# Kernel tuning notes

Hardware: AMD Instinct MI355X
Metric: run time of the kernel (lower is better)

The kernel has to match this reference:

```python
import jax, jax.numpy as jnp
import numpy as np
from jax import lax

SEQ, BSZ = 64, 32
NTOK, NINP, NHID, NLAYERS = 50000, 512, 1024, 2
BN_EPS = 1e-5


def setup_inputs() -> dict:
    key = jax.random.key(0)
    ks = jax.random.split(key, 12)
    s = 0.05
    return {
        "input_ids": jax.random.randint(ks[0], (SEQ, BSZ), 0, NTOK),
        "hx": jnp.zeros((NLAYERS, BSZ, NHID), jnp.float32),
        "cx": jnp.zeros((NLAYERS, BSZ, NHID), jnp.float32),
        "emb_w": jax.random.normal(ks[1], (NTOK, NINP), jnp.float32) * 0.01,
        "Wih0": jax.random.normal(ks[2], (4 * NHID, NINP), jnp.float32) * s,
        "Whh0": jax.random.normal(ks[3], (4 * NHID, NHID), jnp.float32) * s,
        "bih0": jnp.zeros((4 * NHID,), jnp.float32),
        "bhh0": jnp.zeros((4 * NHID,), jnp.float32),
        "Wih1": jax.random.normal(ks[4], (4 * NHID, NHID), jnp.float32) * s,
        "Whh1": jax.random.normal(ks[5], (4 * NHID, NHID), jnp.float32) * s,
        "bih1": jnp.zeros((4 * NHID,), jnp.float32),
        "bhh1": jnp.zeros((4 * NHID,), jnp.float32),
        "Wp": jax.random.normal(ks[6], (NINP, NHID), jnp.float32) * s,
        "bp": jnp.zeros((NINP,), jnp.float32),
        "Wd": jax.random.normal(ks[7], (NTOK, NINP), jnp.float32) * 0.01,
        "bd": jnp.zeros((NTOK,), jnp.float32),
    }


def _lstm_cell(x, h, c, Wih, Whh, bih, bhh):
    # torch.nn.LSTMCell math; gates packed as [i, f, g, o]
    gates = x @ Wih.T + bih + h @ Whh.T + bhh  # [B, 4H]
    i, f, g, o = jnp.split(gates, 4, axis=-1)
    i = jax.nn.sigmoid(i)
    f = jax.nn.sigmoid(f)
    g = jnp.tanh(g)
    o = jax.nn.sigmoid(o)
    c2 = f * c + i * g
    h2 = o * jnp.tanh(c2)
    return h2, c2


def reference(input_ids, hx, cx, emb_w, Wih0, Whh0, bih0, bhh0,
              Wih1, Whh1, bih1, bhh1, Wp, bp, Wd, bd):
    # eval mode: drop / internal_drop / rdrop are identity; rmask == 1
    emb = emb_w[input_ids]  # [S, B, ninp]
    layers = ((Wih0, Whh0, bih0, bhh0), (Wih1, Whh1, bih1, bhh1))

    def step(carry, x_t):
        h, c = carry  # each [nlayers, B, H]
        hi = x_t
        hs, cs = [], []
        for j in range(NLAYERS):
            Wih, Whh, bih, bhh = layers[j]
            hj, cj = _lstm_cell(hi, h[j], c[j], Wih, Whh, bih, bhh)
            hs.append(hj)
            cs.append(cj)
            hi = hj
        return (jnp.stack(hs, 0), jnp.stack(cs, 0)), hi

    (hxf, cxf), out = lax.scan(step, (hx, cx), emb)  # out: [S, B, H]
    flat = out.reshape(-1, NHID)  # [S*B, H]
    # predictor: Linear -> BatchNorm1d (eval: running_mean=0, running_var=1,
    # gamma=1, beta=0) -> Tanh
    pre = flat @ Wp.T + bp
    p = jnp.tanh(pre * (1.0 / jnp.sqrt(jnp.float32(1.0 + BN_EPS))))
    decoded = p @ Wd.T + bd  # [S*B, ntoken]
    return decoded.reshape(SEQ, BSZ, NTOK), (hxf, cxf)
```

## Files before the change

kernel.cpp:

```cpp
#include <hip/hip_runtime.h>
#include <hip/hip_bf16.h>

using bf16 = __hip_bfloat16;
typedef __attribute__((ext_vector_type(8))) short short8;
typedef __attribute__((ext_vector_type(4))) float f32x4;

#define MFMA_BF16(A,B,C) __builtin_amdgcn_mfma_f32_16x16x32_bf16((A),(B),(C),0,0,0)

static __device__ __forceinline__ unsigned bf16bits(float f) {
  union { bf16 h; unsigned short u; } cv; cv.h = __float2bfloat16(f); return cv.u;
}

static __device__ __forceinline__ void gload16(const void* g, void* l) {
  __builtin_amdgcn_global_load_lds(
      (const __attribute__((address_space(1))) void*)g,
      (__attribute__((address_space(3))) void*)l, 16, 0, 0);
}

template<int EPI>
__global__ __launch_bounds__(256)
void gemm_bt(const bf16* __restrict__ A, const bf16* __restrict__ B,
             const float* __restrict__ bias1, const float* __restrict__ bias2,
             float* __restrict__ Cf, bf16* __restrict__ Cb,
             int M, int N, int K, int Nreal)
{
  __shared__ __align__(1024) bf16 As[128*32];
  __shared__ __align__(1024) bf16 Bs[128*32];
  const int tid  = threadIdx.x;
  const int wave = tid >> 6, lane = tid & 63;
  const int wr = wave >> 1, wc = wave & 1;
  const int row0 = blockIdx.y * 128;
  const int col0 = blockIdx.x * 128;

  f32x4 acc[4][4];
  #pragma unroll
  for (int m = 0; m < 4; ++m)
    #pragma unroll
    for (int n = 0; n < 4; ++n) { f32x4 z = {0.f,0.f,0.f,0.f}; acc[m][n] = z; }

  const int r_sub = lane >> 2;
  const int kc    = lane & 3;

  for (int k0 = 0; k0 < K; k0 += 32) {
    __syncthreads();
    #pragma unroll
    for (int j = 0; j < 2; ++j) {
      const int rb = wave*32 + j*16;
      gload16(A + (size_t)(row0 + rb + r_sub)*K + k0 + kc*8,
              (void*)((char*)As + (size_t)rb*64));
      gload16(B + (size_t)(col0 + rb + r_sub)*K + k0 + kc*8,
              (void*)((char*)Bs + (size_t)rb*64));
    }
    __syncthreads();

    short8 af[4], bfv[4];
    #pragma unroll
    for (int m = 0; m < 4; ++m)
      af[m] = *(const short8*)(As + (wr*64 + m*16 + (lane&15))*32 + (lane>>4)*8);
    #pragma unroll
    for (int n = 0; n < 4; ++n)
      bfv[n] = *(const short8*)(Bs + (wc*64 + n*16 + (lane&15))*32 + (lane>>4)*8);
    #pragma unroll
    for (int m = 0; m < 4; ++m)
      #pragma unroll
      for (int n = 0; n < 4; ++n)
        acc[m][n] = MFMA_BF16(af[m], bfv[n], acc[m][n]);
  }

  const float BN_SCALE = 0.9999950000374997f;
  #pragma unroll
  for (int m = 0; m < 4; ++m) {
    const int rg0 = row0 + wr*64 + m*16 + ((lane>>4)<<2);
    #pragma unroll
    for (int n = 0; n < 4; ++n) {
      const int cg = col0 + wc*64 + n*16 + (lane&15);
      if (EPI == 2) {
        const int bq = cg >> 4, q = cg & 15;
        const int orig = (q>>2)*1024 + bq*4 + (q&3);
        const float bb = bias1[orig] + bias2[orig];
        #pragma unroll
        for (int j = 0; j < 4; ++j) {
          const int row = rg0 + j;
          Cf[((size_t)bq*64 + (row>>5))*512 + (size_t)(row&31)*16 + q]
              = acc[m][n][j] + bb;
        }
      } else if (cg < Nreal) {
        float bb = 0.f;
        if (bias1) bb += bias1[cg];
        if (bias2) bb += bias2[cg];
        #pragma unroll
        for (int j = 0; j < 4; ++j) {
          float v = acc[m][n][j] + bb;
          v = tanhf(v * BN_SCALE);
          Cb[(size_t)(rg0+j)*Nreal + cg] = __float2bfloat16(v);
        }
      }
    }
  }
}

__global__ __launch_bounds__(512, 2)
void gemm_dec(const bf16* __restrict__ A, const bf16* __restrict__ B,
              const float* __restrict__ bias, float* __restrict__ C,
              int M, int N, int K, int Nreal)
{
  __shared__ __align__(1024) bf16 As[2*256*32];
  __shared__ __align__(1024) bf16 Bs[2*256*32];
  const int tid  = threadIdx.x;
  const int wave = tid >> 6, lane = tid & 63;
  const int wr = wave >> 2, wc = wave & 3;
  const int row0 = blockIdx.y * 256;
  const int col0 = blockIdx.x * 256;

  f32x4 acc[8][4];
  #pragma unroll
  for (int m = 0; m < 8; ++m)
    #pragma unroll
    for (int n = 0; n < 4; ++n) { f32x4 z = {0.f,0.f,0.f,0.f}; acc[m][n] = z; }

  const int r_sub = lane >> 2;
  const int kc    = lane & 3;

  auto STAGE = [&](int sl, int k0) {
    #pragma unroll
    for (int j = 0; j < 2; ++j) {
      const int rb = wave*32 + j*16;
      gload16(A + (size_t)(row0 + rb + r_sub)*K + k0 + kc*8,
              (void*)((char*)As + (size_t)sl*16384 + (size_t)rb*64));
      gload16(B + (size_t)(col0 + rb + r_sub)*K + k0 + kc*8,
              (void*)((char*)Bs + (size_t)sl*16384 + (size_t)rb*64));
    }
  };

  const int NT = K >> 5;
  STAGE(0, 0);
  if (NT > 1) STAGE(1, 32);

  for (int kk = 0; kk < NT; ++kk) {
    const int cur = kk & 1;
    if (kk == NT - 1) asm volatile("s_waitcnt vmcnt(0)" ::: "memory");
    else              asm volatile("s_waitcnt vmcnt(4)" ::: "memory");
    __builtin_amdgcn_sched_barrier(0);
    __builtin_amdgcn_s_barrier();

    const bf16* Ab = As + (size_t)cur*8192;
    const bf16* Bb = Bs + (size_t)cur*8192;
    short8 af[8], bfv[4];
    #pragma unroll
    for (int m = 0; m < 8; ++m)
      af[m] = *(const short8*)(Ab + (wr*128 + m*16 + (lane&15))*32 + (lane>>4)*8);
    #pragma unroll
    for (int n = 0; n < 4; ++n)
      bfv[n] = *(const short8*)(Bb + (wc*64 + n*16 + (lane&15))*32 + (lane>>4)*8);
    #pragma unroll
    for (int m = 0; m < 8; ++m)
      #pragma unroll
      for (int n = 0; n < 4; ++n)
        acc[m][n] = MFMA_BF16(af[m], bfv[n], acc[m][n]);

    asm volatile("s_waitcnt lgkmcnt(0)" ::: "memory");
    __builtin_amdgcn_sched_barrier(0);
    __builtin_amdgcn_s_barrier();
    if (kk + 2 < NT) STAGE(cur, (kk + 2) * 32);
  }

  #pragma unroll
  for (int m = 0; m < 8; ++m) {
    const int rg0 = row0 + wr*128 + m*16 + ((lane>>4)<<2);
    #pragma unroll
    for (int n = 0; n < 4; ++n) {
      const int cg = col0 + wc*64 + n*16 + (lane&15);
      if (cg < Nreal) {
        const float bb = bias[cg];
        #pragma unroll
        for (int j = 0; j < 4; ++j)
          __builtin_nontemporal_store(acc[m][n][j] + bb,
                                      C + (size_t)(rg0+j)*Nreal + cg);
      }
    }
  }
}

__global__ __launch_bounds__(256, 1)
void k_lstm_persist(const bf16* __restrict__ hinit, const float* __restrict__ cx,
                    const bf16* __restrict__ Wpack, const float* __restrict__ g0p,
                    const float* __restrict__ bih1, const float* __restrict__ bhh1,
                    bf16* __restrict__ h0_all, bf16* __restrict__ h1_all,
                    float* __restrict__ tail, unsigned* __restrict__ flags)
{
  const int b    = blockIdx.x;
  const int tid  = threadIdx.x;
  const int wave = tid >> 6, lane = tid & 63;

  __shared__ __align__(1024) bf16 Wlds[96*512];
  __shared__ float P[4][2][32][20];

  const bf16* wbase = Wpack + (size_t)b * 96 * 512;
  #pragma unroll
  for (int it = 0; it < 24; ++it) {
    const int chunk = it*4 + wave;
    gload16(wbase + (size_t)chunk*512 + lane*8,
            (void*)((char*)Wlds + (size_t)chunk*1024));
  }

  const int layer = tid >> 7;
  const int cell  = tid & 127;
  const int r     = cell >> 2;
  const int hc    = cell & 3;
  const int col   = b*4 + hc;
  float creg = cx[(size_t)layer*32768 + (size_t)r*1024 + col];
  float bsum[4];
  #pragma unroll
  for (int g = 0; g < 4; ++g)
    bsum[g] = (layer == 1) ? (bih1[g*1024 + col] + bhh1[g*1024 + col]) : 0.f;

  const int arow = lane & 15;
  const int koff = (lane >> 4) * 8;

  const unsigned* fp0 = flags + (lane*4+0)*32;
  const unsigned* fp1 = flags + (lane*4+1)*32;
  const unsigned* fp2 = flags + (lane*4+2)*32;
  const unsigned* fp3 = flags + (lane*4+3)*32;

  __syncthreads();

  for (int s = 0; s < 65; ++s) {
    const bf16* hA = (s == 0) ? hinit           : h0_all + (size_t)(s-1)*32768;
    const bf16* hB = (s <= 1) ? (hinit + 32768) : h1_all + (size_t)(s-2)*32768;

    short8 a0[8], a1[8], c0[8], c1[8];
    #pragma unroll
    for (int i = 0; i < 8; ++i) {
      const int kb = wave*256 + i*32 + koff;
      a0[i] = *(const short8*)(hA + (size_t)arow*1024      + kb);
      a1[i] = *(const short8*)(hA + (size_t)(arow+16)*1024 + kb);
      c0[i] = *(const short8*)(hB + (size_t)arow*1024      + kb);
      c1[i] = *(const short8*)(hB + (size_t)(arow+16)*1024 + kb);
    }
    float gpre[4] = {0.f, 0.f, 0.f, 0.f};
    if (layer == 0 && s < 64) {
      const float* gr = g0p + ((size_t)(b*64 + s)*32 + r)*16;
      #pragma unroll
      for (int g = 0; g < 4; ++g) gpre[g] = gr[g*4 + hc];
    }

    f32x4 z = {0.f,0.f,0.f,0.f};
    f32x4 acc00 = z, acc01 = z, acc10 = z, acc11 = z;
    #pragma unroll
    for (int i = 0; i < 8; ++i) {
      const int ks = wave*8 + i;
      short8 w0 = *(const short8*)(Wlds + ((size_t)(     ks)*64 + lane)*8);
      short8 w1 = *(const short8*)(Wlds + ((size_t)(32 + ks)*64 + lane)*8);
      short8 w2 = *(const short8*)(Wlds + ((size_t)(64 + ks)*64 + lane)*8);
      acc00 = MFMA_BF16(a0[i], w0, acc00);
      acc01 = MFMA_BF16(a1[i], w0, acc01);
      acc10 = MFMA_BF16(a0[i], w1, acc10);
      acc11 = MFMA_BF16(a1[i], w1, acc11);
      acc10 = MFMA_BF16(c0[i], w2, acc10);
      acc11 = MFMA_BF16(c1[i], w2, acc11);
    }

    #pragma unroll
    for (int j = 0; j < 4; ++j) {
      const int pr = (lane >> 4)*4 + j;
      P[wave][0][pr     ][lane & 15] = acc00[j];
      P[wave][0][pr + 16][lane & 15] = acc01[j];
      P[wave][1][pr     ][lane & 15] = acc10[j];
      P[wave][1][pr + 16][lane & 15] = acc11[j];
    }
    __syncthreads();

    const int t = s - layer;
    if (t >= 0 && t < 64) {
      float v[4];
      #pragma unroll
      for (int g = 0; g < 4; ++g) {
        const int j = g*4 + hc;
        v[g] = P[0][layer][r][j] + P[1][layer][r][j]
             + P[2][layer][r][j] + P[3][layer][r][j] + bsum[g] + gpre[g];
      }
      const float iv = 1.f/(1.f + expf(-v[0]));
      const float fv = 1.f/(1.f + expf(-v[1]));
      const float gv = tanhf(v[2]);
      const float ov = 1.f/(1.f + expf(-v[3]));
      creg = fv*creg + iv*gv;
      const float hn = ov*tanhf(creg);
      unsigned hu  = bf16bits(hn);
      unsigned p01 = hu | ((unsigned)__shfl_xor((int)hu, 1) << 16);
      unsigned p23 = (unsigned)__shfl_xor((int)p01, 2);
      if (hc == 0) {
        bf16* hp = (layer ? h1_all : h0_all) + (size_t)t*32768 + (size_t)r*1024 + b*4;
        unsigned long long v64 = (unsigned long long)p01
                               | ((unsigned long long)p23 << 32);
        __hip_atomic_store((unsigned long long*)hp, v64,
                           __ATOMIC_RELAXED, __HIP_MEMORY_SCOPE_AGENT);
      }
      if (t == 63) {
        tail[(size_t)layer*32768 + (size_t)r*1024 + col]         = hn;
        tail[65536 + (size_t)layer*32768 + (size_t)r*1024 + col] = creg;
      }
    }
    if (s == 64) break;

    __syncthreads();
    if (tid == 0) {
      asm volatile("global_store_dword %0, %1, off sc0 sc1\n\t"
                   "s_waitcnt vmcnt(0)"
                   :: "v"(flags + b*32), "v"((unsigned)(s + 1)) : "memory");
    }
    if (wave == 0) {
      const unsigned su = (unsigned)s;
      for (;;) {
        unsigned v0, v1, v2, v3;
        asm volatile("global_load_dword %0, %1, off sc0 sc1" : "=v"(v0) : "v"(fp0));
        asm volatile("global_load_dword %0, %1, off sc0 sc1" : "=v"(v1) : "v"(fp1));
        asm volatile("global_load_dword %0, %1, off sc0 sc1" : "=v"(v2) : "v"(fp2));
        asm volatile("global_load_dword %0, %1, off sc0 sc1" : "=v"(v3) : "v"(fp3));
        asm volatile("s_waitcnt vmcnt(0)" ::: "memory");
        bool ok = (v0 > su) & (v1 > su) & (v2 > su) & (v3 > su);
        if (__all(ok)) break;
        __builtin_amdgcn_s_sleep(1);
      }
    }
    __syncthreads();
    asm volatile("" ::: "memory");
    __builtin_amdgcn_sched_barrier(0);
  }
}

__global__ __launch_bounds__(256)
void k_pack(const float* __restrict__ Whh0, const float* __restrict__ Wih1,
            const float* __restrict__ Whh1, bf16* __restrict__ Wpack)
{
  const int b = blockIdx.x;
  #pragma unroll 4
  for (int it = 0; it < 24; ++it) {
    const int idx = it*256 + threadIdx.x;
    const int chunkp = idx >> 6;
    const int l = idx & 63;
    const int p = chunkp >> 5, c = chunkp & 31;
    const float* W = (p == 0) ? Whh0 : (p == 1 ? Wih1 : Whh1);
    const int j = l & 15;
    const int row = (j>>2)*1024 + b*4 + (j&3);
    const int k = c*32 + (l>>4)*8;
    const float* src = W + (size_t)row*1024 + k;
    bf16* dst = Wpack + ((size_t)(b*96 + chunkp)*64 + l)*8;
    #pragma unroll
    for (int q = 0; q < 8; ++q) dst[q] = __float2bfloat16(src[q]);
  }
}

__global__ void k_cvt(const float* __restrict__ s, bf16* __restrict__ d, long n) {
  long i = (long)blockIdx.x*blockDim.x + threadIdx.x;
  if (i < n) d[i] = __float2bfloat16(s[i]);
}

__global__ void k_cvt_perm(const float* __restrict__ src, bf16* __restrict__ dst) {
  const int n = blockIdx.x;
  const int orig = ((n>>2)&3)*1024 + (n>>4)*4 + (n&3);
  const float4 v = ((const float4*)(src + (size_t)orig*512))[threadIdx.x];
  bf16* d = dst + (size_t)n*512 + threadIdx.x*4;
  d[0] = __float2bfloat16(v.x); d[1] = __float2bfloat16(v.y);
  d[2] = __float2bfloat16(v.z); d[3] = __float2bfloat16(v.w);
}

__global__ void k_cvt_pad(const float* __restrict__ s, bf16* __restrict__ d,
                          long n, long nrows_real, int rowlen) {
  long i = (long)blockIdx.x*blockDim.x + threadIdx.x;
  if (i < n) {
    long r = i / rowlen;
    d[i] = (r < nrows_real) ? __float2bfloat16(s[i]) : __float2bfloat16(0.f);
  }
}

__global__ void k_init(const float* __restrict__ hx, bf16* __restrict__ hinit,
                       unsigned* __restrict__ flags) {
  int i = blockIdx.x*blockDim.x + threadIdx.x;
  if (i < 8192) flags[i] = 0u;
  if (i < 65536) hinit[i] = __float2bfloat16(hx[i]);
}

__global__ void k_embed(const int* __restrict__ ids, const float* __restrict__ emb_w,
                        bf16* __restrict__ out) {
  const int row = blockIdx.x;
  const int tok = ids[row];
  const float4 v = ((const float4*)(emb_w + (size_t)tok*512))[threadIdx.x];
  bf16* d = out + (size_t)row*512 + threadIdx.x*4;
  d[0] = __float2bfloat16(v.x); d[1] = __float2bfloat16(v.y);
  d[2] = __float2bfloat16(v.z); d[3] = __float2bfloat16(v.w);
}

extern "C" void kernel_launch(void* const* d_in, const int* in_sizes, int n_in,
                              void* d_out, int out_size, void* d_ws, size_t ws_size,
                              hipStream_t stream) {
  const int*   ids  = (const int*)d_in[0];
  const float* hx   = (const float*)d_in[1];
  const float* cx   = (const float*)d_in[2];
  const float* embw = (const float*)d_in[3];
  const float* Wih0 = (const float*)d_in[4];
  const float* Whh0 = (const float*)d_in[5];
  const float* bih0 = (const float*)d_in[6];
  const float* bhh0 = (const float*)d_in[7];
  const float* Wih1 = (const float*)d_in[8];
  const float* Whh1 = (const float*)d_in[9];
  const float* bih1 = (const float*)d_in[10];
  const float* bhh1 = (const float*)d_in[11];
  const float* Wp   = (const float*)d_in[12];
  const float* bp   = (const float*)d_in[13];
  const float* Wd   = (const float*)d_in[14];
  const float* bd   = (const float*)d_in[15];
  float* out = (float*)d_out;

  char* w = (char*)d_ws;
  bf16* Wih0b = (bf16*)w; w += 4096l*512*2;
  bf16* Wpack = (bf16*)w; w += 256l*96*64*8*2;
  bf16* Wpb   = (bf16*)w; w += 512l*1024*2;
  bf16* Wdb   = (bf16*)w; w += 50176l*512*2;
  bf16* embb  = (bf16*)w; w += 2048l*512*2;
  float* g0p  = (float*)w; w += 2048l*4096*4;
  bf16* h0a   = (bf16*)w; w += 2048l*1024*2;
  bf16* h1a   = (bf16*)w; w += 2048l*1024*2;
  bf16* hinit = (bf16*)w; w += 2l*32*1024*2;
  bf16* pb    = (bf16*)w; w += 2048l*512*2;
  unsigned* flags = (unsigned*)w; w += 8192*4;

  k_cvt_perm<<<4096, 128, 0, stream>>>(Wih0, Wih0b);
  k_cvt<<<(512l*1024 + 255)/256, 256, 0, stream>>>(Wp, Wpb, 512l*1024);
  k_cvt_pad<<<(50176l*512 + 255)/256, 256, 0, stream>>>(Wd, Wdb, 50176l*512, 50000, 512);
  k_init<<<256, 256, 0, stream>>>(hx, hinit, flags);
  k_embed<<<2048, 128, 0, stream>>>(ids, embw, embb);
  k_pack<<<256, 256, 0, stream>>>(Whh0, Wih1, Whh1, Wpack);

  gemm_bt<2><<<dim3(32, 16), 256, 0, stream>>>(
      embb, Wih0b, bih0, bhh0, g0p, nullptr, 2048, 4096, 512, 4096);

  float* tail = out + 102400000l;
  k_lstm_persist<<<256, 256, 0, stream>>>(hinit, cx, Wpack, g0p, bih1, bhh1,
                                          h0a, h1a, tail, flags);

  gemm_bt<1><<<dim3(4, 16), 256, 0, stream>>>(
      h1a, Wpb, bp, nullptr, nullptr, pb, 2048, 512, 1024, 512);

  gemm_dec<<<dim3(196, 8), 512, 0, stream>>>(
      pb, Wdb, bd, out, 2048, 50176, 512, 50000);
}
```

Measured before the change: 713.2 us.

## Fold weight conversions into persistent LSTM kernel to overlap with recurrence

Drops the separate k_pack, k_cvt and k_cvt_pad launches. The persistent LSTM kernel now converts its recurrent weights from fp32 straight into LDS, and at each timestep spreads the conversion of the decoder and projection weights to bf16 across all blocks. This is meant to hide the large Wd conversion behind the latency-bound recurrence and remove the Wpack round trip through memory. The cost is extra global traffic and VALU work inside every recurrent step, which could lengthen the critical path between flag syncs.

```diff
diff --git a/kernel.cpp b/kernel.cpp
--- a/kernel.cpp
+++ b/kernel.cpp
@@ -183,8 +183,11 @@
 
 __global__ __launch_bounds__(256, 1)
 void k_lstm_persist(const bf16* __restrict__ hinit, const float* __restrict__ cx,
-                    const bf16* __restrict__ Wpack, const float* __restrict__ g0p,
+                    const float* __restrict__ Whh0, const float* __restrict__ Wih1,
+                    const float* __restrict__ Whh1, const float* __restrict__ g0p,
                     const float* __restrict__ bih1, const float* __restrict__ bhh1,
+                    const float* __restrict__ Wd, const float* __restrict__ Wp,
+                    bf16* __restrict__ Wdb, bf16* __restrict__ Wpb,
                     bf16* __restrict__ h0_all, bf16* __restrict__ h1_all,
                     float* __restrict__ tail, unsigned* __restrict__ flags)
 {
@@ -195,12 +198,25 @@
   __shared__ __align__(1024) bf16 Wlds[96*512];
   __shared__ float P[4][2][32][20];
 
-  const bf16* wbase = Wpack + (size_t)b * 96 * 512;
   #pragma unroll
   for (int it = 0; it < 24; ++it) {
-    const int chunk = it*4 + wave;
-    gload16(wbase + (size_t)chunk*512 + lane*8,
-            (void*)((char*)Wlds + (size_t)chunk*1024));
+    const int idx = it*256 + tid;
+    const int chunkp = idx >> 6;
+    const int l = idx & 63;
+    const int p = chunkp >> 5, c = chunkp & 31;
+    const float* W = (p == 0) ? Whh0 : (p == 1 ? Wih1 : Whh1);
+    const int j = l & 15;
+    const int row = (j>>2)*1024 + b*4 + (j&3);
+    const int k = c*32 + (l>>4)*8;
+    const float* src = W + (size_t)row*1024 + k;
+    const float4 v0 = *(const float4*)(src);
+    const float4 v1 = *(const float4*)(src + 4);
+    short8 pk;
+    pk[0] = (short)bf16bits(v0.x); pk[1] = (short)bf16bits(v0.y);
+    pk[2] = (short)bf16bits(v0.z); pk[3] = (short)bf16bits(v0.w);
+    pk[4] = (short)bf16bits(v1.x); pk[5] = (short)bf16bits(v1.y);
+    pk[6] = (short)bf16bits(v1.z); pk[7] = (short)bf16bits(v1.w);
+    *(short8*)(Wlds + ((size_t)chunkp*64 + l)*8) = pk;
   }
 
   const int layer = tid >> 7;
@@ -300,6 +316,31 @@
         tail[65536 + (size_t)layer*32768 + (size_t)r*1024 + col] = creg;
       }
     }
+
+    if (s < 64) {
+      const long base = (((long)s*256 + b)*256 + tid)*2;
+      #pragma unroll
+      for (int uu = 0; uu < 2; ++uu) {
+        const long u = base + uu;
+        if (u < 6422528) {
+          const long e = u*4;
+          const int row = (int)(e >> 9);
+          float4 v = (row < 50000) ? *(const float4*)(Wd + e)
+                                   : make_float4(0.f,0.f,0.f,0.f);
+          unsigned lo = bf16bits(v.x) | (bf16bits(v.y) << 16);
+          unsigned hi = bf16bits(v.z) | (bf16bits(v.w) << 16);
+          uint2 pkd; pkd.x = lo; pkd.y = hi;
+          *(uint2*)(Wdb + e) = pkd;
+        } else if (u < 6553600) {
+          const long e = (u - 6422528)*4;
+          float4 v = *(const float4*)(Wp + e);
+          unsigned lo = bf16bits(v.x) | (bf16bits(v.y) << 16);
+          unsigned hi = bf16bits(v.z) | (bf16bits(v.w) << 16);
+          uint2 pkd; pkd.x = lo; pkd.y = hi;
+          *(uint2*)(Wpb + e) = pkd;
+        }
+      }
+    }
     if (s == 64) break;
 
     __syncthreads();
@@ -328,33 +369,6 @@
   }
 }
 
-__global__ __launch_bounds__(256)
-void k_pack(const float* __restrict__ Whh0, const float* __restrict__ Wih1,
-            const float* __restrict__ Whh1, bf16* __restrict__ Wpack)
-{
-  const int b = blockIdx.x;
-  #pragma unroll 4
-  for (int it = 0; it < 24; ++it) {
-    const int idx = it*256 + threadIdx.x;
-    const int chunkp = idx >> 6;
-    const int l = idx & 63;
-    const int p = chunkp >> 5, c = chunkp & 31;
-    const float* W = (p == 0) ? Whh0 : (p == 1 ? Wih1 : Whh1);
-    const int j = l & 15;
-    const int row = (j>>2)*1024 + b*4 + (j&3);
-    const int k = c*32 + (l>>4)*8;
-    const float* src = W + (size_t)row*1024 + k;
-    bf16* dst = Wpack + ((size_t)(b*96 + chunkp)*64 + l)*8;
-    #pragma unroll
-    for (int q = 0; q < 8; ++q) dst[q] = __float2bfloat16(src[q]);
-  }
-}
-
-__global__ void k_cvt(const float* __restrict__ s, bf16* __restrict__ d, long n) {
-  long i = (long)blockIdx.x*blockDim.x + threadIdx.x;
-  if (i < n) d[i] = __float2bfloat16(s[i]);
-}
-
 __global__ void k_cvt_perm(const float* __restrict__ src, bf16* __restrict__ dst) {
   const int n = blockIdx.x;
   const int orig = ((n>>2)&3)*1024 + (n>>4)*4 + (n&3);
@@ -362,15 +376,6 @@
   bf16* d = dst + (size_t)n*512 + threadIdx.x*4;
   d[0] = __float2bfloat16(v.x); d[1] = __float2bfloat16(v.y);
   d[2] = __float2bfloat16(v.z); d[3] = __float2bfloat16(v.w);
-}
-
-__global__ void k_cvt_pad(const float* __restrict__ s, bf16* __restrict__ d,
-                          long n, long nrows_real, int rowlen) {
-  long i = (long)blockIdx.x*blockDim.x + threadIdx.x;
-  if (i < n) {
-    long r = i / rowlen;
-    d[i] = (r < nrows_real) ? __float2bfloat16(s[i]) : __float2bfloat16(0.f);
-  }
 }
 
 __global__ void k_init(const float* __restrict__ hx, bf16* __restrict__ hinit,
@@ -413,7 +418,6 @@
 
   char* w = (char*)d_ws;
   bf16* Wih0b = (bf16*)w; w += 4096l*512*2;
-  bf16* Wpack = (bf16*)w; w += 256l*96*64*8*2;
   bf16* Wpb   = (bf16*)w; w += 512l*1024*2;
   bf16* Wdb   = (bf16*)w; w += 50176l*512*2;
   bf16* embb  = (bf16*)w; w += 2048l*512*2;
@@ -425,17 +429,15 @@
   unsigned* flags = (unsigned*)w; w += 8192*4;
 
   k_cvt_perm<<<4096, 128, 0, stream>>>(Wih0, Wih0b);
-  k_cvt<<<(512l*1024 + 255)/256, 256, 0, stream>>>(Wp, Wpb, 512l*1024);
-  k_cvt_pad<<<(50176l*512 + 255)/256, 256, 0, stream>>>(Wd, Wdb, 50176l*512, 50000, 512);
   k_init<<<256, 256, 0, stream>>>(hx, hinit, flags);
   k_embed<<<2048, 128, 0, stream>>>(ids, embw, embb);
-  k_pack<<<256, 256, 0, stream>>>(Whh0, Wih1, Whh1, Wpack);
 
   gemm_bt<2><<<dim3(32, 16), 256, 0, stream>>>(
       embb, Wih0b, bih0, bhh0, g0p, nullptr, 2048, 4096, 512, 4096);
 
   float* tail = out + 102400000l;
-  k_lstm_persist<<<256, 256, 0, stream>>>(hinit, cx, Wpack, g0p, bih1, bhh1,
+  k_lstm_persist<<<256, 256, 0, stream>>>(hinit, cx, Whh0, Wih1, Whh1, g0p,
+                                          bih1, bhh1, Wd, Wp, Wdb, Wpb,
                                           h0a, h1a, tail, flags);
 
   gemm_bt<1><<<dim3(4, 16), 256, 0, stream>>>(
```

After: 720.4 us. Within noise of the previous version (+1.0%).
